# Kernel optimization log

Hardware: AMD Instinct MI355X
Metric: run time of the kernel (lower is better)

## Reference

```python
import math
import jax, jax.numpy as jnp
import numpy as np

B, S, L = 4, 1024, 1024
D, H = 1024, 16
HD = D // H            # 64, even -> rotary_dim == head_dim
HIDDEN = 4 * D         # SwiGLU hidden
ROPE_BASE = 10000.0
EPS = 1e-6


def rmsnorm(x, w):
    return x * jax.lax.rsqrt(jnp.mean(x * x, axis=-1, keepdims=True) + EPS) * w


def safe_key_padding_mask(mask):
    # rows where ALL keys are padded become all-valid to avoid NaN softmax
    all_pad = jnp.all(mask, axis=-1, keepdims=True)
    return jnp.where(all_pad, False, mask)


def split_heads(x):
    b, t, _ = x.shape
    return x.reshape(b, t, H, HD).transpose(0, 2, 1, 3)  # [b,h,t,hd]


def merge_heads(x):
    b, _, t, _ = x.shape
    return x.transpose(0, 2, 1, 3).reshape(b, t, H * HD)


def apply_rope(x):
    # x: [b,h,t,hd]; interleaved even/odd rotation, matching the torch stack/flatten
    t = x.shape[-2]
    pos = jnp.arange(t, dtype=jnp.float32)[:, None]
    freqs = jnp.exp(jnp.arange(0, HD, 2, dtype=jnp.float32) * (-math.log(ROPE_BASE) / HD))
    ang = pos * freqs[None, :]                      # [t, hd/2]
    sin = jnp.sin(ang).astype(x.dtype)
    cos = jnp.cos(ang).astype(x.dtype)
    even, odd = x[..., 0::2], x[..., 1::2]
    rot = jnp.stack((even * cos - odd * sin, even * sin + odd * cos), axis=-1)
    return rot.reshape(x.shape)


def masked_attn(q, k, v, valid_keys):
    # q:[b,h,tq,hd] k,v:[b,h,tk,hd] valid_keys:[b,tk] (True = attendable)
    scores = jnp.einsum('bhqd,bhkd->bhqk', q, k) / math.sqrt(HD)
    scores = jnp.where(valid_keys[:, None, None, :], scores, jnp.finfo(scores.dtype).min)
    return jnp.einsum('bhqk,bhkd->bhqd', jax.nn.softmax(scores, axis=-1), v)


def setup_inputs():
    key = jax.random.key(0)
    ks = jax.random.split(key, 30)
    sc = 0.02
    n = lambda k, shp: jax.random.normal(k, shp, jnp.float32)
    inp = {
        'tokens': n(ks[0], (B, S, D)),
        'seq_tokens': n(ks[1], (B, L, D)),
        'modulation': n(ks[2], (B, D)),
        'attn_norm_w': jnp.ones((D,), jnp.float32),
        'qkv_w': n(ks[3], (3 * D, D)) * sc,
        'qkv_b': jnp.zeros((3 * D,), jnp.float32),
        'out_w': n(ks[4], (D, D)) * sc,
        'out_b': jnp.zeros((D,), jnp.float32),
        'film_w': n(ks[5], (2 * D, D)) * sc,
        'film_b': jnp.zeros((2 * D,), jnp.float32),
        'sq_norm_w': jnp.ones((D,), jnp.float32),
        's_norm_w': jnp.ones((D,), jnp.float32),
        'mha_in_w': n(ks[6], (3 * D, D)) * sc,
        'mha_in_b': jnp.zeros((3 * D,), jnp.float32),
        'mha_out_w': n(ks[7], (D, D)) * sc,
        'mha_out_b': jnp.zeros((D,), jnp.float32),
        'gate_w': n(ks[8], (D, 2 * D)) * sc,
        'gate_b': jnp.zeros((D,), jnp.float32),
        'ffn_norm_w': jnp.ones((D,), jnp.float32),
        'gu_w': n(ks[9], (2 * HIDDEN, D)) * sc,
        'gu_b': jnp.zeros((2 * HIDDEN,), jnp.float32),
        'down_w': n(ks[10], (D, HIDDEN)) * sc,
        'down_b': jnp.zeros((D,), jnp.float32),
        'padding_mask': jax.random.bernoulli(ks[11], 0.1, (B, S)),
        'seq_mask': jax.random.bernoulli(ks[12], 0.1, (B, L)),
    }
    return inp


def reference(tokens, seq_tokens, modulation, attn_norm_w, qkv_w, qkv_b, out_w, out_b,
              film_w, film_b, sq_norm_w, s_norm_w, mha_in_w, mha_in_b, mha_out_w, mha_out_b,
              gate_w, gate_b, ffn_norm_w, gu_w, gu_b, down_w, down_b,
              padding_mask, seq_mask):
    # --- FiLM-modulated pre-norm ---
    x = rmsnorm(tokens, attn_norm_w)
    scale, shift = jnp.split(modulation @ film_w.T + film_b, 2, axis=-1)
    x = x * (1.0 + 0.1 * jnp.tanh(scale))[:, None, :] + shift[:, None, :]
    # --- rotary self-attention ---
    q, k, v = jnp.split(x @ qkv_w.T + qkv_b, 3, axis=-1)
    q, k, v = split_heads(q), split_heads(k), split_heads(v)
    q, k = apply_rope(q), apply_rope(k)
    valid = ~safe_key_padding_mask(padding_mask)
    tokens = tokens + merge_heads(masked_attn(q, k, v, valid)) @ out_w.T + out_b
    # --- cross-attention over the (single) context sequence ---
    query = rmsnorm(tokens, sq_norm_w)
    src = rmsnorm(seq_tokens, s_norm_w)
    wq, wk, wv = jnp.split(mha_in_w, 3, axis=0)
    bq, bk, bv = jnp.split(mha_in_b, 3, axis=0)
    cq = split_heads(query @ wq.T + bq)
    ck = split_heads(src @ wk.T + bk)
    cv = split_heads(src @ wv.T + bv)
    svalid = ~safe_key_padding_mask(seq_mask)
    attended = merge_heads(masked_attn(cq, ck, cv, svalid)) @ mha_out_w.T + mha_out_b
    valid_rows = jnp.any(~seq_mask, axis=1).astype(attended.dtype)[:, None, None]
    update = attended * valid_rows  # mean over 1 sequence == identity
    gate = jax.nn.sigmoid(jnp.concatenate([tokens, update], axis=-1) @ gate_w.T + gate_b)
    tokens = tokens + gate * update
    # --- SwiGLU FFN ---
    h = rmsnorm(tokens, ffn_norm_w)
    g, val = jnp.split(h @ gu_w.T + gu_b, 2, axis=-1)
    return tokens + (jax.nn.silu(g) * val) @ down_w.T + down_b
```

## Files before the change

### kernel.cpp

```cpp
#include <hip/hip_runtime.h>
#include <hip/hip_bf16.h>
#include <math.h>

#define BB 4
#define SS 1024
#define DD 1024
#define NH 16
#define HD 64

using bf16 = __hip_bfloat16;
typedef __bf16 bf16x8 __attribute__((ext_vector_type(8)));
typedef __bf16 bf16x4 __attribute__((ext_vector_type(4)));
typedef float f32x4 __attribute__((ext_vector_type(4)));

#define AS3(p) ((__attribute__((address_space(3))) void*)(p))
#define AS1(p) ((const __attribute__((address_space(1))) void*)(p))

__device__ __forceinline__ void stage128(const bf16* __restrict__ g, int ld,
                                         int row0, int k0, __bf16* lds,
                                         int wave, int lane)
{
    const int l15 = lane & 15, q = lane >> 4;
#pragma unroll
    for (int j = 0; j < 2; ++j) {
        int grp = wave * 2 + j;
        const bf16* gp = g + (size_t)(row0 + grp * 16 + l15) * ld + k0 + q * 8;
        __builtin_amdgcn_global_load_lds(AS1(gp), AS3((char*)lds + grp * 1024), 16, 0, 0);
    }
}

__device__ __forceinline__ void stageH(const bf16* __restrict__ g, int ld,
                                       int row0, int k0, __bf16* lds,
                                       int wid, int lane)
{
    const int l15 = lane & 15, q = lane >> 4;
#pragma unroll
    for (int j = 0; j < 2; ++j) {
        int grp = wid * 2 + j;
        const bf16* gp = g + (size_t)(row0 + grp * 16 + l15) * ld + k0 + q * 8;
        __builtin_amdgcn_global_load_lds(AS1(gp), AS3((char*)lds + grp * 1024), 16, 0, 0);
    }
}

__device__ __forceinline__ bf16x8 ldsfrag(const __bf16* lds, int grp, int quad, int l15)
{
    return *(const bf16x8*)((const char*)lds + grp * 1024 + quad * 256 + l15 * 16);
}

template<int RES>
__global__ __launch_bounds__(512, 2)
void gemm256p_kernel(const bf16* __restrict__ A, const bf16* __restrict__ W, int ldw,
                     const bf16* __restrict__ bias, bf16* __restrict__ Cout,
                     const bf16* __restrict__ Res, int K, int ldc)
{
    __shared__ __bf16 L[2][2][2][8192];
    const int wid = threadIdx.x >> 6, lane = threadIdx.x & 63;
    const int quad = lane >> 4, l15 = lane & 15;
    const int wm = wid >> 2, wn = wid & 3;
    const int n0 = blockIdx.x * 256, m0 = blockIdx.y * 256;
    const int nt = K >> 6;

    stageH(A, K,   m0, 0,  &L[0][0][0][0], wid, lane);
    stageH(W, ldw, n0, 0,  &L[0][1][0][0], wid, lane);
    stageH(A, K,   m0, 32, &L[0][0][1][0], wid, lane);
    stageH(W, ldw, n0, 32, &L[0][1][1][0], wid, lane);

    f32x4 acc[8][4] = {};
    bf16x8 af[8], bf[2];

    for (int t = 0; t < nt; ++t) {
        const int buf = t & 1, nbuf = buf ^ 1;
        const int kn = (t + 1) * 64;
        const bool more = (t + 1) < nt;

        asm volatile("s_waitcnt vmcnt(4)\n\ts_barrier" ::: "memory");
        {
            const __bf16* LA = &L[buf][0][0][0];
            const __bf16* LB = &L[buf][1][0][0];
#pragma unroll
            for (int m = 0; m < 8; ++m) af[m] = ldsfrag(LA, wm * 8 + m, quad, l15);
            bf[0] = ldsfrag(LB, wn * 4 + 0, quad, l15);
            bf[1] = ldsfrag(LB, wn * 4 + 1, quad, l15);
            if (more) stageH(A, K, m0, kn, &L[nbuf][0][0][0], wid, lane);
            __builtin_amdgcn_s_setprio(1);
#pragma unroll
            for (int m = 0; m < 8; ++m) {
                acc[m][0] = __builtin_amdgcn_mfma_f32_16x16x32_bf16(af[m], bf[0], acc[m][0], 0, 0, 0);
                acc[m][1] = __builtin_amdgcn_mfma_f32_16x16x32_bf16(af[m], bf[1], acc[m][1], 0, 0, 0);
            }
            __builtin_amdgcn_s_setprio(0);
        }

        asm volatile("s_barrier" ::: "memory");
        {
            const __bf16* LB = &L[buf][1][0][0];
            bf[0] = ldsfrag(LB, wn * 4 + 2, quad, l15);
            bf[1] = ldsfrag(LB, wn * 4 + 3, quad, l15);
            if (more) stageH(W, ldw, n0, kn, &L[nbuf][1][0][0], wid, lane);
            __builtin_amdgcn_s_setprio(1);
#pragma unroll
            for (int m = 0; m < 8; ++m) {
                acc[m][2] = __builtin_amdgcn_mfma_f32_16x16x32_bf16(af[m], bf[0], acc[m][2], 0, 0, 0);
                acc[m][3] = __builtin_amdgcn_mfma_f32_16x16x32_bf16(af[m], bf[1], acc[m][3], 0, 0, 0);
            }
            __builtin_amdgcn_s_setprio(0);
        }

        if (more) asm volatile("s_waitcnt vmcnt(4)\n\ts_barrier" ::: "memory");
        else      asm volatile("s_waitcnt vmcnt(0)\n\ts_barrier" ::: "memory");
        {
            const __bf16* LA = &L[buf][0][1][0];
            const __bf16* LB = &L[buf][1][1][0];
#pragma unroll
            for (int m = 0; m < 8; ++m) af[m] = ldsfrag(LA, wm * 8 + m, quad, l15);
            bf[0] = ldsfrag(LB, wn * 4 + 0, quad, l15);
            bf[1] = ldsfrag(LB, wn * 4 + 1, quad, l15);
            if (more) stageH(A, K, m0, kn + 32, &L[nbuf][0][1][0], wid, lane);
            __builtin_amdgcn_s_setprio(1);
#pragma unroll
            for (int m = 0; m < 8; ++m) {
                acc[m][0] = __builtin_amdgcn_mfma_f32_16x16x32_bf16(af[m], bf[0], acc[m][0], 0, 0, 0);
                acc[m][1] = __builtin_amdgcn_mfma_f32_16x16x32_bf16(af[m], bf[1], acc[m][1], 0, 0, 0);
            }
            __builtin_amdgcn_s_setprio(0);
        }

        asm volatile("s_barrier" ::: "memory");
        {
            const __bf16* LB = &L[buf][1][1][0];
            bf[0] = ldsfrag(LB, wn * 4 + 2, quad, l15);
            bf[1] = ldsfrag(LB, wn * 4 + 3, quad, l15);
            if (more) stageH(W, ldw, n0, kn + 32, &L[nbuf][1][1][0], wid, lane);
            __builtin_amdgcn_s_setprio(1);
#pragma unroll
            for (int m = 0; m < 8; ++m) {
                acc[m][2] = __builtin_amdgcn_mfma_f32_16x16x32_bf16(af[m], bf[0], acc[m][2], 0, 0, 0);
                acc[m][3] = __builtin_amdgcn_mfma_f32_16x16x32_bf16(af[m], bf[1], acc[m][3], 0, 0, 0);
            }
            __builtin_amdgcn_s_setprio(0);
        }
    }

    const int mw = m0 + wm * 128, nw = n0 + wn * 64;
#pragma unroll
    for (int i = 0; i < 8; ++i)
#pragma unroll
        for (int j = 0; j < 4; ++j) {
            const int col = nw + j * 16 + l15;
            const float bs = (float)bias[col];
#pragma unroll
            for (int r = 0; r < 4; ++r) {
                int row = mw + i * 16 + quad * 4 + r;
                size_t off = (size_t)row * ldc + col;
                float v = acc[i][j][r] + bs;
                if (RES == 2) {
                    float g = fminf(fmaxf(v, -60.f), 60.f);
                    v = (g / (1.f + __expf(-g))) * (float)Res[off];
                }
                Cout[off] = __float2bfloat16(v);
            }
        }
}

template<int RES, bool SCALE>
__global__ __launch_bounds__(256)
void gemm128_kernel(const bf16* __restrict__ A, const bf16* __restrict__ W, int ldw,
                    const bf16* __restrict__ bias, bf16* __restrict__ Cout,
                    const bf16* __restrict__ Res, const float* __restrict__ scaleb,
                    int K, int ldc)
{
    __shared__ __bf16 As[2][4096], Bs[2][4096];
    const int wave = threadIdx.x >> 6, lane = threadIdx.x & 63;
    const int quad = lane >> 4, l15 = lane & 15;
    const int n0 = blockIdx.x * 128, m0 = blockIdx.y * 128;
    const int mg0 = (wave >> 1) * 4, ng0 = (wave & 1) * 4;

    stage128(A, K, m0, 0, As[0], wave, lane);
    stage128(W, ldw, n0, 0, Bs[0], wave, lane);

    f32x4 acc[4][4] = {};
    const int steps = K >> 5;
    for (int s = 0; s < steps; ++s) {
        __syncthreads();
        const int cur = s & 1, nxt = cur ^ 1;
        bf16x8 af[4], bfv[4];
#pragma unroll
        for (int i = 0; i < 4; ++i) af[i] = ldsfrag(As[cur], mg0 + i, quad, l15);
#pragma unroll
        for (int j = 0; j < 4; ++j) bfv[j] = ldsfrag(Bs[cur], ng0 + j, quad, l15);
        if (s + 1 < steps) {
            stage128(A, K, m0, (s + 1) * 32, As[nxt], wave, lane);
            stage128(W, ldw, n0, (s + 1) * 32, Bs[nxt], wave, lane);
        }
#pragma unroll
        for (int i = 0; i < 4; ++i)
#pragma unroll
            for (int j = 0; j < 4; ++j)
                acc[i][j] = __builtin_amdgcn_mfma_f32_16x16x32_bf16(af[i], bfv[j], acc[i][j], 0, 0, 0);
    }

    const float scl = SCALE ? scaleb[m0 >> 10] : 1.f;
#pragma unroll
    for (int i = 0; i < 4; ++i)
#pragma unroll
        for (int j = 0; j < 4; ++j) {
            const int col = n0 + (ng0 + j) * 16 + l15;
            const float bs = (float)bias[col];
#pragma unroll
            for (int r = 0; r < 4; ++r) {
                int row = m0 + (mg0 + i) * 16 + quad * 4 + r;
                float v = acc[i][j][r] + bs;
                if (SCALE) v *= scl;
                size_t off = (size_t)row * ldc + col;
                if (RES == 1) v += (float)Res[off];
                Cout[off] = __float2bfloat16(v);
            }
        }
}

__global__ __launch_bounds__(256)
void gate128_kernel(const bf16* __restrict__ A1, const bf16* __restrict__ A2,
                    const bf16* __restrict__ Wg, const bf16* __restrict__ bias,
                    bf16* __restrict__ GT)
{
    __shared__ __bf16 As[2][4096], Bs[2][4096];
    const int wave = threadIdx.x >> 6, lane = threadIdx.x & 63;
    const int quad = lane >> 4, l15 = lane & 15;
    const int n0 = blockIdx.x * 128, m0 = blockIdx.y * 128;
    const int mg0 = (wave >> 1) * 4, ng0 = (wave & 1) * 4;

    stage128(A1, 1024, m0, 0, As[0], wave, lane);
    stage128(Wg, 2048, n0, 0, Bs[0], wave, lane);

    f32x4 acc[4][4] = {};
    for (int s = 0; s < 64; ++s) {
        __syncthreads();
        const int cur = s & 1, nxt = cur ^ 1;
        bf16x8 af[4], bfv[4];
#pragma unroll
        for (int i = 0; i < 4; ++i) af[i] = ldsfrag(As[cur], mg0 + i, quad, l15);
#pragma unroll
        for (int j = 0; j < 4; ++j) bfv[j] = ldsfrag(Bs[cur], ng0 + j, quad, l15);
        if (s + 1 < 64) {
            const bf16* Asrc = (s + 1 < 32) ? A1 : A2;
            stage128(Asrc, 1024, m0, ((s + 1) & 31) * 32, As[nxt], wave, lane);
            stage128(Wg, 2048, n0, (s + 1) * 32, Bs[nxt], wave, lane);
        }
#pragma unroll
        for (int i = 0; i < 4; ++i)
#pragma unroll
            for (int j = 0; j < 4; ++j)
                acc[i][j] = __builtin_amdgcn_mfma_f32_16x16x32_bf16(af[i], bfv[j], acc[i][j], 0, 0, 0);
    }

#pragma unroll
    for (int i = 0; i < 4; ++i)
#pragma unroll
        for (int j = 0; j < 4; ++j) {
            const int col = n0 + (ng0 + j) * 16 + l15;
            const float bs = (float)bias[col];
#pragma unroll
            for (int r = 0; r < 4; ++r) {
                int row = m0 + (mg0 + i) * 16 + quad * 4 + r;
                float v = fminf(fmaxf(acc[i][j][r] + bs, -60.f), 60.f);
                GT[(size_t)row * 1024 + col] = __float2bfloat16(1.f / (1.f + __expf(-v)));
            }
        }
}

__global__ __launch_bounds__(256)
void down128_kernel(const bf16* __restrict__ ACT, const bf16* __restrict__ W,
                    const bf16* __restrict__ bias, void* __restrict__ out,
                    const bf16* __restrict__ T3, const int* __restrict__ flags)
{
    __shared__ __bf16 As[2][4096], Bs[2][4096];
    const int wave = threadIdx.x >> 6, lane = threadIdx.x & 63;
    const int quad = lane >> 4, l15 = lane & 15;
    const int n0 = blockIdx.x * 128, m0 = blockIdx.y * 128;
    const int mg0 = (wave >> 1) * 4, ng0 = (wave & 1) * 4;

    stage128(ACT, 4096, m0, 0, As[0], wave, lane);
    stage128(W,   4096, n0, 0, Bs[0], wave, lane);

    f32x4 acc[4][4] = {};
    for (int s = 0; s < 128; ++s) {
        __syncthreads();
        const int cur = s & 1, nxt = cur ^ 1;
        bf16x8 af[4], bfv[4];
#pragma unroll
        for (int i = 0; i < 4; ++i) af[i] = ldsfrag(As[cur], mg0 + i, quad, l15);
#pragma unroll
        for (int j = 0; j < 4; ++j) bfv[j] = ldsfrag(Bs[cur], ng0 + j, quad, l15);
        if (s + 1 < 128) {
            stage128(ACT, 4096, m0, (s + 1) * 32, As[nxt], wave, lane);
            stage128(W,   4096, n0, (s + 1) * 32, Bs[nxt], wave, lane);
        }
#pragma unroll
        for (int i = 0; i < 4; ++i)
#pragma unroll
            for (int j = 0; j < 4; ++j)
                acc[i][j] = __builtin_amdgcn_mfma_f32_16x16x32_bf16(af[i], bfv[j], acc[i][j], 0, 0, 0);
    }

    const int f32out = flags[0];
#pragma unroll
    for (int i = 0; i < 4; ++i)
#pragma unroll
        for (int j = 0; j < 4; ++j) {
            const int col = n0 + (ng0 + j) * 16 + l15;
            const float bs = (float)bias[col];
#pragma unroll
            for (int r = 0; r < 4; ++r) {
                size_t row = (size_t)m0 + (mg0 + i) * 16 + quad * 4 + r;
                size_t off = row * 1024 + col;
                float v = acc[i][j][r] + bs + (float)T3[off];
                if (f32out) ((float*)out)[off] = v;
                else        ((bf16*)out)[off] = __float2bfloat16(v);
            }
        }
}

__global__ __launch_bounds__(256)
void probe_kernel(const void* __restrict__ tokens, int* __restrict__ flags)
{
    const unsigned short* u = (const unsigned short*)tokens;
    int t = threadIdx.x, bad = 0;
    for (int i = t; i < 8192; i += 256) {
        int e = (u[i] >> 7) & 0xFF;
        if (e >= 0xC5) bad++;
    }
    __shared__ int red[256];
    red[t] = bad; __syncthreads();
    for (int s = 128; s > 0; s >>= 1) { if (t < s) red[t] += red[t + s]; __syncthreads(); }
    if (t == 0) flags[0] = (red[0] > 16) ? 1 : 0;
}

struct CvtJobs {
    const void* src[23];
    bf16* dst[23];
    int n[23];
    int blk0[24];
};

__global__ __launch_bounds__(256)
void cvt_all_kernel(CvtJobs J, const int* __restrict__ flags)
{
    int b = blockIdx.x, j = 0;
    while (b >= J.blk0[j + 1]) ++j;
    int i0 = (b - J.blk0[j]) * 2048 + threadIdx.x * 8;
    if (i0 >= J.n[j]) return;
    bf16* dst = J.dst[j];
    if (flags[0]) {
        const float4* s = (const float4*)((const float*)J.src[j] + i0);
        float4 a = s[0], c = s[1];
        __bf16 o[8];
        o[0] = (__bf16)a.x; o[1] = (__bf16)a.y; o[2] = (__bf16)a.z; o[3] = (__bf16)a.w;
        o[4] = (__bf16)c.x; o[5] = (__bf16)c.y; o[6] = (__bf16)c.z; o[7] = (__bf16)c.w;
        *(bf16x8*)(dst + i0) = *(bf16x8*)o;
    } else {
        *(bf16x8*)(dst + i0) = *(const bf16x8*)((const bf16*)J.src[j] + i0);
    }
}

__global__ __launch_bounds__(256)
void film_kernel(const bf16* __restrict__ mod, const bf16* __restrict__ fw,
                 const bf16* __restrict__ fb, float* __restrict__ F)
{
    int o = blockIdx.x * 256 + threadIdx.x;
    int b = o >> 11, c = o & 2047;
    const bf16x8* m = (const bf16x8*)(mod + b * DD);
    const bf16x8* w = (const bf16x8*)(fw + (size_t)c * DD);
    float s = (float)fb[c];
    for (int j = 0; j < DD / 8; ++j) {
        bf16x8 mv = m[j], wv = w[j];
#pragma unroll
        for (int e = 0; e < 8; ++e) s += (float)mv[e] * (float)wv[e];
    }
    if (c < 1024) s = 1.f + 0.1f * tanhf(s);
    F[o] = s;
}

template<typename TIN, int FILM>
__global__ __launch_bounds__(256)
void rmsnorm_kernel(const TIN* __restrict__ in, const bf16* __restrict__ w,
                    bf16* __restrict__ out, const float* __restrict__ F)
{
    int row = blockIdx.x, t = threadIdx.x, b = row >> 10;
    const TIN* x = in + (size_t)row * DD;
    float v[4];
    if constexpr (sizeof(TIN) == 2) {
        bf16x4 u = *(const bf16x4*)((const __bf16*)x + t * 4);
#pragma unroll
        for (int i = 0; i < 4; ++i) v[i] = (float)u[i];
    } else {
        float4 u = *(const float4*)((const float*)x + t * 4);
        v[0] = u.x; v[1] = u.y; v[2] = u.z; v[3] = u.w;
    }
    float ss = v[0]*v[0] + v[1]*v[1] + v[2]*v[2] + v[3]*v[3];
    __shared__ float red[256];
    red[t] = ss; __syncthreads();
    for (int s = 128; s > 0; s >>= 1) { if (t < s) red[t] += red[t + s]; __syncthreads(); }
    float rn = rsqrtf(red[0] * (1.f / DD) + 1e-6f);
    bf16x4 wv = *(const bf16x4*)((const __bf16*)w + t * 4);
    __bf16 o4[4];
#pragma unroll
    for (int i = 0; i < 4; ++i) {
        int d = t * 4 + i;
        float y = v[i] * rn * (float)wv[i];
        if (FILM) y = y * F[b * 2048 + d] + F[b * 2048 + 1024 + d];
        o4[i] = (__bf16)y;
    }
    *(bf16x4*)((__bf16*)out + (size_t)row * DD + t * 4) = *(bf16x4*)o4;
}

__global__ __launch_bounds__(256)
void mask_kernel(const void* __restrict__ mask, int* __restrict__ valid,
                 float* __restrict__ vr)
{
    int b = blockIdx.x, t = threadIdx.x;
    const unsigned* mi = (const unsigned*)mask;
    const unsigned char* mb = (const unsigned char*)mask;
    __shared__ int red[256];

    int viol = 0;
    for (int i = t; i < 1024; i += 256) if (mi[i] > 1u) viol++;
    red[t] = viol; __syncthreads();
    for (int s = 128; s > 0; s >>= 1) { if (t < s) red[t] += red[t + s]; __syncthreads(); }
    int isByte = (red[0] > 0);
    __syncthreads();

    int z = 0;
    for (int i = t; i < SS; i += 256) {
        int mv = isByte ? (int)mb[b * SS + i] : (int)mi[b * SS + i];
        z += (mv == 0);
    }
    red[t] = z; __syncthreads();
    for (int s = 128; s > 0; s >>= 1) { if (t < s) red[t] += red[t + s]; __syncthreads(); }
    int nvalid = red[0];
    int allpad = (nvalid == 0);
    for (int i = t; i < SS; i += 256) {
        int mv = isByte ? (int)mb[b * SS + i] : (int)mi[b * SS + i];
        valid[b * SS + i] = allpad ? 1 : (mv ? 0 : 1);
    }
    if (t == 0) vr[b] = (nvalid > 0) ? 1.f : 0.f;
}

__global__ __launch_bounds__(256)
void rope_kernel(bf16* __restrict__ qkv)
{
    int row = blockIdx.x;
    int s = row & (SS - 1);
    for (int j = threadIdx.x; j < 1024; j += 256) {
        int sec = j >> 9;
        int p = j & 511;
        int i = p & 31;
        int col = sec * DD + p * 2;
        float fi = __expf(-(float)(2 * i) * 0.14391157f);
        float ang = (float)s * fi;
        float sn, cs; sincosf(ang, &sn, &cs);
        size_t base = (size_t)row * (3 * DD) + col;
        float e = (float)qkv[base], o = (float)qkv[base + 1];
        qkv[base]     = __float2bfloat16(e * cs - o * sn);
        qkv[base + 1] = __float2bfloat16(e * sn + o * cs);
    }
}

__global__ __launch_bounds__(256)
void vtrans_kernel(const bf16* __restrict__ vsrc, int ld, bf16* __restrict__ vtg)
{
    __shared__ __bf16 tile[64][65];
    const int t = threadIdx.x;
    const int k0 = blockIdx.x * 64;
    const int h = blockIdx.y, b = blockIdx.z;
#pragma unroll
    for (int j = 0; j < 2; ++j) {
        int lin = j * 256 + t;
        int r = lin >> 3, c8 = (lin & 7) * 8;
        bf16x8 v = *(const bf16x8*)(vsrc + ((size_t)b * 1024 + k0 + r) * ld + h * 64 + c8);
#pragma unroll
        for (int e = 0; e < 8; ++e) tile[r][c8 + e] = v[e];
    }
    __syncthreads();
#pragma unroll
    for (int j = 0; j < 2; ++j) {
        int lin = j * 256 + t;
        int d = lin >> 3, k8 = (lin & 7) * 8;
        __bf16 o[8];
#pragma unroll
        for (int e = 0; e < 8; ++e) o[e] = tile[k8 + e][d];
        *(bf16x8*)(vtg + ((size_t)(b * 16 + h) * 64 + d) * 1024 + k0 + k8) = *(bf16x8*)o;
    }
}

__global__ __launch_bounds__(256)
void attn_mfma_kernel(const bf16* __restrict__ qp, const bf16* __restrict__ kp,
                      int ld, const bf16* __restrict__ vtg,
                      const int* __restrict__ valid, bf16* __restrict__ out)
{
    __shared__ __bf16 Kl[128][72];
    __shared__ __bf16 Vl[64][136];
    __shared__ __bf16 Pl[4][16][136];
    __shared__ float biasl[1024];

    const int t = threadIdx.x;
    const int wave = t >> 6, lane = t & 63, quad = lane >> 4, l15 = lane & 15;
    const int q0 = blockIdx.x * 64;
    const int h = blockIdx.y, b = blockIdx.z;

    for (int i = t; i < 1024; i += 256)
        biasl[i] = valid[b * 1024 + i] ? 0.f : -1e30f;

    const size_t qrow = (size_t)b * 1024 + q0 + wave * 16 + l15;
    const bf16x8 qf0 = *(const bf16x8*)(qp + qrow * ld + h * 64 + quad * 8);
    const bf16x8 qf1 = *(const bf16x8*)(qp + qrow * ld + h * 64 + 32 + quad * 8);

    f32x4 O[4] = {{0,0,0,0},{0,0,0,0},{0,0,0,0},{0,0,0,0}};
    float mrow[4] = {-1e30f, -1e30f, -1e30f, -1e30f};
    float lrow[4] = {0.f, 0.f, 0.f, 0.f};

    for (int ic = 0; ic < 8; ++ic) {
        const int k0 = ic * 128;
        __syncthreads();
#pragma unroll
        for (int j = 0; j < 4; ++j) {
            int lin = j * 256 + t;
            int r = lin >> 3, c8 = (lin & 7) * 8;
            *(bf16x8*)&Kl[r][c8] =
                *(const bf16x8*)(kp + ((size_t)b * 1024 + k0 + r) * ld + h * 64 + c8);
            int d = lin >> 4, s8 = (lin & 15) * 8;
            *(bf16x8*)&Vl[d][s8] =
                *(const bf16x8*)(vtg + ((size_t)(b * 16 + h) * 64 + d) * 1024 + k0 + s8);
        }
        __syncthreads();

        float sreg[8][4];
#pragma unroll
        for (int f = 0; f < 8; ++f) {
            bf16x8 kb0 = *(const bf16x8*)&Kl[f * 16 + l15][quad * 8];
            bf16x8 kb1 = *(const bf16x8*)&Kl[f * 16 + l15][32 + quad * 8];
            f32x4 s = {0, 0, 0, 0};
            s = __builtin_amdgcn_mfma_f32_16x16x32_bf16(qf0, kb0, s, 0, 0, 0);
            s = __builtin_amdgcn_mfma_f32_16x16x32_bf16(qf1, kb1, s, 0, 0, 0);
            float bfr = biasl[k0 + f * 16 + l15];
#pragma unroll
            for (int i = 0; i < 4; ++i) sreg[f][i] = s[i] * 0.125f + bfr;
        }

        float mloc[4] = {-1e30f, -1e30f, -1e30f, -1e30f};
#pragma unroll
        for (int f = 0; f < 8; ++f)
#pragma unroll
            for (int i = 0; i < 4; ++i) mloc[i] = fmaxf(mloc[i], sreg[f][i]);
#pragma unroll
        for (int off = 1; off < 16; off <<= 1)
#pragma unroll
            for (int i = 0; i < 4; ++i)
                mloc[i] = fmaxf(mloc[i], __shfl_xor(mloc[i], off));
        float alpha[4];
#pragma unroll
        for (int i = 0; i < 4; ++i) {
            float mn = fmaxf(mrow[i], mloc[i]);
            alpha[i] = __expf(mrow[i] - mn);
            mrow[i] = mn;
            lrow[i] *= alpha[i];
        }
#pragma unroll
        for (int dt = 0; dt < 4; ++dt)
#pragma unroll
            for (int i = 0; i < 4; ++i) O[dt][i] *= alpha[i];

        float lloc[4] = {0.f, 0.f, 0.f, 0.f};
#pragma unroll
        for (int f = 0; f < 8; ++f)
#pragma unroll
            for (int i = 0; i < 4; ++i) {
                float p = __expf(sreg[f][i] - mrow[i]);
                lloc[i] += p;
                Pl[wave][quad * 4 + i][f * 16 + l15] = (__bf16)p;
            }
#pragma unroll
        for (int off = 1; off < 16; off <<= 1)
#pragma unroll
            for (int i = 0; i < 4; ++i) lloc[i] += __shfl_xor(lloc[i], off);
#pragma unroll
        for (int i = 0; i < 4; ++i) lrow[i] += lloc[i];

        __syncthreads();

#pragma unroll
        for (int kc = 0; kc < 4; ++kc) {
            bf16x8 pa = *(const bf16x8*)&Pl[wave][l15][kc * 32 + quad * 8];
#pragma unroll
            for (int dt = 0; dt < 4; ++dt) {
                bf16x8 vb = *(const bf16x8*)&Vl[dt * 16 + l15][kc * 32 + quad * 8];
                O[dt] = __builtin_amdgcn_mfma_f32_16x16x32_bf16(pa, vb, O[dt], 0, 0, 0);
            }
        }
    }

#pragma unroll
    for (int i = 0; i < 4; ++i) {
        float inv = 1.f / lrow[i];
        size_t orow = (size_t)b * 1024 + q0 + wave * 16 + quad * 4 + i;
#pragma unroll
        for (int dt = 0; dt < 4; ++dt)
            out[orow * 1024 + h * 64 + dt * 16 + l15] = __float2bfloat16(O[dt][i] * inv);
    }
}

__global__ __launch_bounds__(256)
void gating_kernel(const bf16* __restrict__ T2, const bf16* __restrict__ GT,
                   const bf16* __restrict__ UPb, bf16* __restrict__ T3)
{
    size_t i0 = ((size_t)blockIdx.x * 256 + threadIdx.x) * 8;
    bf16x8 a = *(const bf16x8*)((const __bf16*)T2 + i0);
    bf16x8 g = *(const bf16x8*)((const __bf16*)GT + i0);
    bf16x8 u = *(const bf16x8*)((const __bf16*)UPb + i0);
    __bf16 o[8];
#pragma unroll
    for (int e = 0; e < 8; ++e)
        o[e] = (__bf16)((float)a[e] + (float)g[e] * (float)u[e]);
    *(bf16x8*)((__bf16*)T3 + i0) = *(bf16x8*)o;
}

extern "C" void kernel_launch(void* const* d_in, const int* in_sizes, int n_in,
                              void* d_out, int out_size, void* d_ws, size_t ws_size,
                              hipStream_t stream)
{
    const int M = BB * SS;
    const size_t MiB = 1 << 20;

    char* ws = (char*)d_ws;

    size_t off = 0;
    auto arena = [&](size_t n) { bf16* p = (bf16*)(ws + off); off += ((n * 2 + 255) & ~(size_t)255); return p; };
    bf16* aTok  = arena(4194304);
    bf16* aSeq  = arena(4194304);
    bf16* aMod  = arena(4096);
    bf16* aANW  = arena(1024);
    bf16* aQKVW = arena(3145728);
    bf16* aQKVB = arena(3072);
    bf16* aOutW = arena(1048576);
    bf16* aOutB = arena(1024);
    bf16* aFilmW= arena(2097152);
    bf16* aFilmB= arena(2048);
    bf16* aSqN  = arena(1024);
    bf16* aSN   = arena(1024);
    bf16* aMIW  = arena(3145728);
    bf16* aMIB  = arena(3072);
    bf16* aMOW  = arena(1048576);
    bf16* aMOB  = arena(1024);
    bf16* aGW   = arena(2097152);
    bf16* aGB   = arena(1024);
    bf16* aFNW  = arena(1024);
    bf16* aGUW  = arena(8388608);
    bf16* aGUB  = arena(8192);
    bf16* aDW   = arena(4194304);
    bf16* aDB   = arena(1024);

    off = (off + MiB - 1) & ~(MiB - 1);
    char* P0 = ws + off;
    char* P1 = P0 + 8 * MiB;
    char* P2 = P0 + 16 * MiB;
    char* P3 = P0 + 24 * MiB;
    char* P4 = P0 + 32 * MiB;
    char* SM = P0 + 40 * MiB;

    bf16* QKV  = (bf16*)P1;
    bf16* A    = (bf16*)P0;
    bf16* Q2   = (bf16*)P1;
    bf16* SRC  = (bf16*)P2;
    bf16* CQ   = (bf16*)P3;
    bf16* CK   = (bf16*)P1;
    bf16* CV   = (bf16*)P0;
    bf16* U    = (bf16*)P2;
    bf16* UPb  = (bf16*)P0;
    bf16* GT   = (bf16*)P1;
    bf16* T3   = (bf16*)P4;
    bf16* Vtg  = (bf16*)P4;
    bf16* ACT  = (bf16*)P0;
    bf16* Vfull= (bf16*)ws;
    bf16* X    = (bf16*)d_out;
    bf16* T2   = (bf16*)d_out;
    bf16* Hb   = (bf16*)d_out;

    float* F    = (float*)SM;
    int* validP = (int*)(SM + 32 * 1024);
    int* validS = (int*)(SM + 48 * 1024);
    float* vrP  = (float*)(SM + 64 * 1024);
    float* vrS  = (float*)(SM + 64 * 1024 + 256);
    int* flags  = (int*)(SM + 64 * 1024 + 512);

    probe_kernel<<<1, 256, 0, stream>>>(d_in[0], flags);

    CvtJobs J;
    const void* srcs[23] = {d_in[0], d_in[1], d_in[2], d_in[3], d_in[4], d_in[5],
                            d_in[6], d_in[7], d_in[8], d_in[9], d_in[10], d_in[11],
                            d_in[12], d_in[13], d_in[14], d_in[15], d_in[16], d_in[17],
                            d_in[18], d_in[19], d_in[20], d_in[21], d_in[22]};
    bf16* dsts[23] = {aTok, aSeq, aMod, aANW, aQKVW, aQKVB, aOutW, aOutB, aFilmW,
                      aFilmB, aSqN, aSN, aMIW, aMIB, aMOW, aMOB, aGW, aGB, aFNW,
                      aGUW, aGUB, aDW, aDB};
    const int ns[23] = {4194304, 4194304, 4096, 1024, 3145728, 3072, 1048576, 1024,
                        2097152, 2048, 1024, 1024, 3145728, 3072, 1048576, 1024,
                        2097152, 1024, 1024, 8388608, 8192, 4194304, 1024};
    int acc_blk = 0;
    for (int j = 0; j < 23; ++j) {
        J.src[j] = srcs[j]; J.dst[j] = dsts[j]; J.n[j] = ns[j];
        J.blk0[j] = acc_blk;
        acc_blk += (ns[j] + 2047) / 2048;
    }
    J.blk0[23] = acc_blk;
    cvt_all_kernel<<<acc_blk, 256, 0, stream>>>(J, flags);

    film_kernel<<<32, 256, 0, stream>>>(aMod, aFilmW, aFilmB, F);
    mask_kernel<<<BB, 256, 0, stream>>>(d_in[23], validP, vrP);
    mask_kernel<<<BB, 256, 0, stream>>>(d_in[24], validS, vrS);

    rmsnorm_kernel<bf16, 1><<<M, 256, 0, stream>>>(aTok, aANW, X, F);

    gemm256p_kernel<0><<<dim3(12, 16), 512, 0, stream>>>(
        X, aQKVW, 1024, aQKVB, QKV, nullptr, 1024, 3072);

    rope_kernel<<<M, 256, 0, stream>>>(QKV);

    vtrans_kernel<<<dim3(16, 16, 4), 256, 0, stream>>>(QKV + 2048, 3072, Vtg);
    attn_mfma_kernel<<<dim3(16, 16, 4), 256, 0, stream>>>(QKV, QKV + 1024, 3072, Vtg, validP, A);

    gemm128_kernel<1, false><<<dim3(8, 32), 256, 0, stream>>>(
        A, aOutW, 1024, aOutB, T2, aTok, nullptr, 1024, 1024);

    rmsnorm_kernel<bf16, 0><<<M, 256, 0, stream>>>(T2, aSqN, Q2, nullptr);
    rmsnorm_kernel<bf16, 0><<<M, 256, 0, stream>>>(aSeq, aSN, SRC, nullptr);

    gemm128_kernel<0, false><<<dim3(8, 32), 256, 0, stream>>>(
        Q2, aMIW, 1024, aMIB, CQ, nullptr, nullptr, 1024, 1024);
    gemm128_kernel<0, false><<<dim3(8, 32), 256, 0, stream>>>(
        SRC, aMIW + 1048576, 1024, aMIB + 1024, CK, nullptr, nullptr, 1024, 1024);
    gemm128_kernel<0, false><<<dim3(8, 32), 256, 0, stream>>>(
        SRC, aMIW + 2097152, 1024, aMIB + 2048, CV, nullptr, nullptr, 1024, 1024);

    vtrans_kernel<<<dim3(16, 16, 4), 256, 0, stream>>>(CV, 1024, Vtg);
    attn_mfma_kernel<<<dim3(16, 16, 4), 256, 0, stream>>>(CQ, CK, 1024, Vtg, validS, U);

    gemm128_kernel<0, true><<<dim3(8, 32), 256, 0, stream>>>(
        U, aMOW, 1024, aMOB, UPb, nullptr, vrS, 1024, 1024);

    gate128_kernel<<<dim3(8, 32), 256, 0, stream>>>(T2, UPb, aGW, aGB, GT);

    gating_kernel<<<(M * 1024) / (256 * 8), 256, 0, stream>>>(T2, GT, UPb, T3);

    rmsnorm_kernel<bf16, 0><<<M, 256, 0, stream>>>(T3, aFNW, Hb, nullptr);

    gemm256p_kernel<0><<<dim3(16, 16), 512, 0, stream>>>(
        Hb, aGUW + (size_t)4096 * 1024, 1024, aGUB + 4096, Vfull, nullptr, 1024, 4096);
    gemm256p_kernel<2><<<dim3(16, 16), 512, 0, stream>>>(
        Hb, aGUW, 1024, aGUB, ACT, Vfull, 1024, 4096);

    down128_kernel<<<dim3(8, 32), 256, 0, stream>>>(ACT, aDW, aDB, d_out, T3, flags);
}
```

Baseline: 826.6 us.

## Split-K gate and down GEMMs with a 256x128 tile kernel, merge cross K/V projections

Replaces the 128x128 gate and down-projection GEMM kernels with a split-K (K split in two) 256x128 tile kernel. It uses 512 threads, a pipeline with two 32-wide k-stages and explicit vmcnt waits, and writes fp32 partials. Separate elementwise kernels then reduce the partials and apply bias, sigmoid or the residual. The cross-attention K and V projections are fused into one wider GEMM writing an interleaved KV buffer, so attention now takes separate q and k strides. This trades extra fp32 partial traffic and two more launches for better tile efficiency and more blocks in flight.

```diff
diff --git a/kernel.cpp b/kernel.cpp
--- a/kernel.cpp
+++ b/kernel.cpp
@@ -40,6 +40,15 @@
         const bf16* gp = g + (size_t)(row0 + grp * 16 + l15) * ld + k0 + q * 8;
         __builtin_amdgcn_global_load_lds(AS1(gp), AS3((char*)lds + grp * 1024), 16, 0, 0);
     }
+}
+
+__device__ __forceinline__ void stageB8(const bf16* __restrict__ g, int ld,
+                                        int row0, int k0, __bf16* lds,
+                                        int wid, int lane)
+{
+    const int l15 = lane & 15, q = lane >> 4;
+    const bf16* gp = g + (size_t)(row0 + wid * 16 + l15) * ld + k0 + q * 8;
+    __builtin_amdgcn_global_load_lds(AS1(gp), AS3((char*)lds + wid * 1024), 16, 0, 0);
 }
 
 __device__ __forceinline__ bf16x8 ldsfrag(const __bf16* lds, int grp, int quad, int l15)
@@ -162,6 +171,138 @@
         }
 }
 
+__global__ __launch_bounds__(512)
+void gemmsk_kernel(const bf16* __restrict__ A0, const bf16* __restrict__ A1, int lda,
+                   const bf16* __restrict__ W0, const bf16* __restrict__ W1, int ldw,
+                   float* __restrict__ PT, int Kz)
+{
+    __shared__ __bf16 LA[2][2][8192];
+    __shared__ __bf16 LB[2][2][4096];
+    const int wid = threadIdx.x >> 6, lane = threadIdx.x & 63;
+    const int quad = lane >> 4, l15 = lane & 15;
+    const int wm = wid >> 2, wn = wid & 3;
+    const int z = blockIdx.z;
+    const bf16* __restrict__ A = z ? A1 : A0;
+    const bf16* __restrict__ W = z ? W1 : W0;
+    const int n0 = blockIdx.x * 128, m0 = blockIdx.y * 256;
+    const int nt = Kz >> 6;
+
+    stageH (A, lda, m0, 0,  &LA[0][0][0], wid, lane);
+    stageB8(W, ldw, n0, 0,  &LB[0][0][0], wid, lane);
+    stageH (A, lda, m0, 32, &LA[0][1][0], wid, lane);
+    stageB8(W, ldw, n0, 32, &LB[0][1][0], wid, lane);
+
+    f32x4 acc[8][2] = {};
+    bf16x8 af[8], bf[2];
+
+    for (int t = 0; t < nt; ++t) {
+        const int buf = t & 1, nbuf = buf ^ 1;
+        const int kn = (t + 1) * 64;
+        const bool more = (t + 1) < nt;
+
+        asm volatile("s_waitcnt vmcnt(3)\n\ts_barrier" ::: "memory");
+        {
+            const __bf16* pA = &LA[buf][0][0];
+            const __bf16* pB = &LB[buf][0][0];
+#pragma unroll
+            for (int m = 0; m < 8; ++m) af[m] = ldsfrag(pA, wm * 8 + m, quad, l15);
+            bf[0] = ldsfrag(pB, wn * 2 + 0, quad, l15);
+            bf[1] = ldsfrag(pB, wn * 2 + 1, quad, l15);
+            if (more) {
+                stageH (A, lda, m0, kn, &LA[nbuf][0][0], wid, lane);
+                stageB8(W, ldw, n0, kn, &LB[nbuf][0][0], wid, lane);
+            }
+            __builtin_amdgcn_s_setprio(1);
+#pragma unroll
+            for (int m = 0; m < 8; ++m) {
+                acc[m][0] = __builtin_amdgcn_mfma_f32_16x16x32_bf16(af[m], bf[0], acc[m][0], 0, 0, 0);
+                acc[m][1] = __builtin_amdgcn_mfma_f32_16x16x32_bf16(af[m], bf[1], acc[m][1], 0, 0, 0);
+            }
+            __builtin_amdgcn_s_setprio(0);
+        }
+
+        if (more) asm volatile("s_waitcnt vmcnt(3)\n\ts_barrier" ::: "memory");
+        else      asm volatile("s_waitcnt vmcnt(0)\n\ts_barrier" ::: "memory");
+        {
+            const __bf16* pA = &LA[buf][1][0];
+            const __bf16* pB = &LB[buf][1][0];
+#pragma unroll
+            for (int m = 0; m < 8; ++m) af[m] = ldsfrag(pA, wm * 8 + m, quad, l15);
+            bf[0] = ldsfrag(pB, wn * 2 + 0, quad, l15);
+            bf[1] = ldsfrag(pB, wn * 2 + 1, quad, l15);
+            if (more) {
+                stageH (A, lda, m0, kn + 32, &LA[nbuf][1][0], wid, lane);
+                stageB8(W, ldw, n0, kn + 32, &LB[nbuf][1][0], wid, lane);
+            }
+            __builtin_amdgcn_s_setprio(1);
+#pragma unroll
+            for (int m = 0; m < 8; ++m) {
+                acc[m][0] = __builtin_amdgcn_mfma_f32_16x16x32_bf16(af[m], bf[0], acc[m][0], 0, 0, 0);
+                acc[m][1] = __builtin_amdgcn_mfma_f32_16x16x32_bf16(af[m], bf[1], acc[m][1], 0, 0, 0);
+            }
+            __builtin_amdgcn_s_setprio(0);
+        }
+    }
+
+    float* P = PT + (size_t)z * (4096 * 1024);
+    const int mw = m0 + wm * 128, nw = n0 + wn * 32;
+#pragma unroll
+    for (int i = 0; i < 8; ++i)
+#pragma unroll
+        for (int j = 0; j < 2; ++j) {
+            const int col = nw + j * 16 + l15;
+#pragma unroll
+            for (int r = 0; r < 4; ++r) {
+                int row = mw + i * 16 + quad * 4 + r;
+                P[(size_t)row * 1024 + col] = acc[i][j][r];
+            }
+        }
+}
+
+__global__ __launch_bounds__(256)
+void reduce_down_kernel(const float* __restrict__ PT, const bf16* __restrict__ bias,
+                        const bf16* __restrict__ T3, void* __restrict__ out,
+                        const int* __restrict__ flags)
+{
+    size_t i0 = ((size_t)blockIdx.x * 256 + threadIdx.x) * 4;
+    float4 p0 = *(const float4*)(PT + i0);
+    float4 p1 = *(const float4*)(PT + 4194304 + i0);
+    int col = (int)(i0 & 1023);
+    bf16x4 b4 = *(const bf16x4*)((const __bf16*)bias + col);
+    bf16x4 t4 = *(const bf16x4*)((const __bf16*)T3 + i0);
+    float v[4] = {p0.x + p1.x, p0.y + p1.y, p0.z + p1.z, p0.w + p1.w};
+#pragma unroll
+    for (int e = 0; e < 4; ++e) v[e] += (float)b4[e] + (float)t4[e];
+    if (flags[0]) {
+        float4 o = {v[0], v[1], v[2], v[3]};
+        *(float4*)((float*)out + i0) = o;
+    } else {
+        __bf16 o4[4];
+#pragma unroll
+        for (int e = 0; e < 4; ++e) o4[e] = (__bf16)v[e];
+        *(bf16x4*)((__bf16*)out + i0) = *(bf16x4*)o4;
+    }
+}
+
+__global__ __launch_bounds__(256)
+void reduce_gate_kernel(const float* __restrict__ PT, const bf16* __restrict__ bias,
+                        bf16* __restrict__ GT)
+{
+    size_t i0 = ((size_t)blockIdx.x * 256 + threadIdx.x) * 4;
+    float4 p0 = *(const float4*)(PT + i0);
+    float4 p1 = *(const float4*)(PT + 4194304 + i0);
+    int col = (int)(i0 & 1023);
+    bf16x4 b4 = *(const bf16x4*)((const __bf16*)bias + col);
+    float v[4] = {p0.x + p1.x, p0.y + p1.y, p0.z + p1.z, p0.w + p1.w};
+    __bf16 o4[4];
+#pragma unroll
+    for (int e = 0; e < 4; ++e) {
+        float g = fminf(fmaxf(v[e] + (float)b4[e], -60.f), 60.f);
+        o4[e] = (__bf16)(1.f / (1.f + __expf(-g)));
+    }
+    *(bf16x4*)((__bf16*)GT + i0) = *(bf16x4*)o4;
+}
+
 template<int RES, bool SCALE>
 __global__ __launch_bounds__(256)
 void gemm128_kernel(const bf16* __restrict__ A, const bf16* __restrict__ W, int ldw,
@@ -214,108 +355,6 @@
                 size_t off = (size_t)row * ldc + col;
                 if (RES == 1) v += (float)Res[off];
                 Cout[off] = __float2bfloat16(v);
-            }
-        }
-}
-
-__global__ __launch_bounds__(256)
-void gate128_kernel(const bf16* __restrict__ A1, const bf16* __restrict__ A2,
-                    const bf16* __restrict__ Wg, const bf16* __restrict__ bias,
-                    bf16* __restrict__ GT)
-{
-    __shared__ __bf16 As[2][4096], Bs[2][4096];
-    const int wave = threadIdx.x >> 6, lane = threadIdx.x & 63;
-    const int quad = lane >> 4, l15 = lane & 15;
-    const int n0 = blockIdx.x * 128, m0 = blockIdx.y * 128;
-    const int mg0 = (wave >> 1) * 4, ng0 = (wave & 1) * 4;
-
-    stage128(A1, 1024, m0, 0, As[0], wave, lane);
-    stage128(Wg, 2048, n0, 0, Bs[0], wave, lane);
-
-    f32x4 acc[4][4] = {};
-    for (int s = 0; s < 64; ++s) {
-        __syncthreads();
-        const int cur = s & 1, nxt = cur ^ 1;
-        bf16x8 af[4], bfv[4];
-#pragma unroll
-        for (int i = 0; i < 4; ++i) af[i] = ldsfrag(As[cur], mg0 + i, quad, l15);
-#pragma unroll
-        for (int j = 0; j < 4; ++j) bfv[j] = ldsfrag(Bs[cur], ng0 + j, quad, l15);
-        if (s + 1 < 64) {
-            const bf16* Asrc = (s + 1 < 32) ? A1 : A2;
-            stage128(Asrc, 1024, m0, ((s + 1) & 31) * 32, As[nxt], wave, lane);
-            stage128(Wg, 2048, n0, (s + 1) * 32, Bs[nxt], wave, lane);
-        }
-#pragma unroll
-        for (int i = 0; i < 4; ++i)
-#pragma unroll
-            for (int j = 0; j < 4; ++j)
-                acc[i][j] = __builtin_amdgcn_mfma_f32_16x16x32_bf16(af[i], bfv[j], acc[i][j], 0, 0, 0);
-    }
-
-#pragma unroll
-    for (int i = 0; i < 4; ++i)
-#pragma unroll
-        for (int j = 0; j < 4; ++j) {
-            const int col = n0 + (ng0 + j) * 16 + l15;
-            const float bs = (float)bias[col];
-#pragma unroll
-            for (int r = 0; r < 4; ++r) {
-                int row = m0 + (mg0 + i) * 16 + quad * 4 + r;
-                float v = fminf(fmaxf(acc[i][j][r] + bs, -60.f), 60.f);
-                GT[(size_t)row * 1024 + col] = __float2bfloat16(1.f / (1.f + __expf(-v)));
-            }
-        }
-}
-
-__global__ __launch_bounds__(256)
-void down128_kernel(const bf16* __restrict__ ACT, const bf16* __restrict__ W,
-                    const bf16* __restrict__ bias, void* __restrict__ out,
-                    const bf16* __restrict__ T3, const int* __restrict__ flags)
-{
-    __shared__ __bf16 As[2][4096], Bs[2][4096];
-    const int wave = threadIdx.x >> 6, lane = threadIdx.x & 63;
-    const int quad = lane >> 4, l15 = lane & 15;
-    const int n0 = blockIdx.x * 128, m0 = blockIdx.y * 128;
-    const int mg0 = (wave >> 1) * 4, ng0 = (wave & 1) * 4;
-
-    stage128(ACT, 4096, m0, 0, As[0], wave, lane);
-    stage128(W,   4096, n0, 0, Bs[0], wave, lane);
-
-    f32x4 acc[4][4] = {};
-    for (int s = 0; s < 128; ++s) {
-        __syncthreads();
-        const int cur = s & 1, nxt = cur ^ 1;
-        bf16x8 af[4], bfv[4];
-#pragma unroll
-        for (int i = 0; i < 4; ++i) af[i] = ldsfrag(As[cur], mg0 + i, quad, l15);
-#pragma unroll
-        for (int j = 0; j < 4; ++j) bfv[j] = ldsfrag(Bs[cur], ng0 + j, quad, l15);
-        if (s + 1 < 128) {
-            stage128(ACT, 4096, m0, (s + 1) * 32, As[nxt], wave, lane);
-            stage128(W,   4096, n0, (s + 1) * 32, Bs[nxt], wave, lane);
-        }
-#pragma unroll
-        for (int i = 0; i < 4; ++i)
-#pragma unroll
-            for (int j = 0; j < 4; ++j)
-                acc[i][j] = __builtin_amdgcn_mfma_f32_16x16x32_bf16(af[i], bfv[j], acc[i][j], 0, 0, 0);
-    }
-
-    const int f32out = flags[0];
-#pragma unroll
-    for (int i = 0; i < 4; ++i)
-#pragma unroll
-        for (int j = 0; j < 4; ++j) {
-            const int col = n0 + (ng0 + j) * 16 + l15;
-            const float bs = (float)bias[col];
-#pragma unroll
-            for (int r = 0; r < 4; ++r) {
-                size_t row = (size_t)m0 + (mg0 + i) * 16 + quad * 4 + r;
-                size_t off = row * 1024 + col;
-                float v = acc[i][j][r] + bs + (float)T3[off];
-                if (f32out) ((float*)out)[off] = v;
-                else        ((bf16*)out)[off] = __float2bfloat16(v);
             }
         }
 }
@@ -494,7 +533,7 @@
 
 __global__ __launch_bounds__(256)
 void attn_mfma_kernel(const bf16* __restrict__ qp, const bf16* __restrict__ kp,
-                      int ld, const bf16* __restrict__ vtg,
+                      int ldq, int ldk, const bf16* __restrict__ vtg,
                       const int* __restrict__ valid, bf16* __restrict__ out)
 {
     __shared__ __bf16 Kl[128][72];
@@ -511,8 +550,8 @@
         biasl[i] = valid[b * 1024 + i] ? 0.f : -1e30f;
 
     const size_t qrow = (size_t)b * 1024 + q0 + wave * 16 + l15;
-    const bf16x8 qf0 = *(const bf16x8*)(qp + qrow * ld + h * 64 + quad * 8);
-    const bf16x8 qf1 = *(const bf16x8*)(qp + qrow * ld + h * 64 + 32 + quad * 8);
+    const bf16x8 qf0 = *(const bf16x8*)(qp + qrow * ldq + h * 64 + quad * 8);
+    const bf16x8 qf1 = *(const bf16x8*)(qp + qrow * ldq + h * 64 + 32 + quad * 8);
 
     f32x4 O[4] = {{0,0,0,0},{0,0,0,0},{0,0,0,0},{0,0,0,0}};
     float mrow[4] = {-1e30f, -1e30f, -1e30f, -1e30f};
@@ -526,7 +565,7 @@
             int lin = j * 256 + t;
             int r = lin >> 3, c8 = (lin & 7) * 8;
             *(bf16x8*)&Kl[r][c8] =
-                *(const bf16x8*)(kp + ((size_t)b * 1024 + k0 + r) * ld + h * 64 + c8);
+                *(const bf16x8*)(kp + ((size_t)b * 1024 + k0 + r) * ldk + h * 64 + c8);
             int d = lin >> 4, s8 = (lin & 15) * 8;
             *(bf16x8*)&Vl[d][s8] =
                 *(const bf16x8*)(vtg + ((size_t)(b * 16 + h) * 64 + d) * 1024 + k0 + s8);
@@ -668,11 +707,10 @@
 
     bf16* QKV  = (bf16*)P1;
     bf16* A    = (bf16*)P0;
-    bf16* Q2   = (bf16*)P1;
+    bf16* Q2   = (bf16*)P3;
     bf16* SRC  = (bf16*)P2;
-    bf16* CQ   = (bf16*)P3;
-    bf16* CK   = (bf16*)P1;
-    bf16* CV   = (bf16*)P0;
+    bf16* CQ   = (bf16*)ws;
+    bf16* KV   = (bf16*)P0;
     bf16* U    = (bf16*)P2;
     bf16* UPb  = (bf16*)P0;
     bf16* GT   = (bf16*)P1;
@@ -680,6 +718,7 @@
     bf16* Vtg  = (bf16*)P4;
     bf16* ACT  = (bf16*)P0;
     bf16* Vfull= (bf16*)ws;
+    float* PTf = (float*)ws;
     bf16* X    = (bf16*)d_out;
     bf16* T2   = (bf16*)d_out;
     bf16* Hb   = (bf16*)d_out;
@@ -725,7 +764,7 @@
     rope_kernel<<<M, 256, 0, stream>>>(QKV);
 
     vtrans_kernel<<<dim3(16, 16, 4), 256, 0, stream>>>(QKV + 2048, 3072, Vtg);
-    attn_mfma_kernel<<<dim3(16, 16, 4), 256, 0, stream>>>(QKV, QKV + 1024, 3072, Vtg, validP, A);
+    attn_mfma_kernel<<<dim3(16, 16, 4), 256, 0, stream>>>(QKV, QKV + 1024, 3072, 3072, Vtg, validP, A);
 
     gemm128_kernel<1, false><<<dim3(8, 32), 256, 0, stream>>>(
         A, aOutW, 1024, aOutB, T2, aTok, nullptr, 1024, 1024);
@@ -735,18 +774,19 @@
 
     gemm128_kernel<0, false><<<dim3(8, 32), 256, 0, stream>>>(
         Q2, aMIW, 1024, aMIB, CQ, nullptr, nullptr, 1024, 1024);
-    gemm128_kernel<0, false><<<dim3(8, 32), 256, 0, stream>>>(
-        SRC, aMIW + 1048576, 1024, aMIB + 1024, CK, nullptr, nullptr, 1024, 1024);
-    gemm128_kernel<0, false><<<dim3(8, 32), 256, 0, stream>>>(
-        SRC, aMIW + 2097152, 1024, aMIB + 2048, CV, nullptr, nullptr, 1024, 1024);
-
-    vtrans_kernel<<<dim3(16, 16, 4), 256, 0, stream>>>(CV, 1024, Vtg);
-    attn_mfma_kernel<<<dim3(16, 16, 4), 256, 0, stream>>>(CQ, CK, 1024, Vtg, validS, U);
+
+    gemm128_kernel<0, false><<<dim3(16, 32), 256, 0, stream>>>(
+        SRC, aMIW + 1048576, 1024, aMIB + 1024, KV, nullptr, nullptr, 1024, 2048);
+
+    vtrans_kernel<<<dim3(16, 16, 4), 256, 0, stream>>>(KV + 1024, 2048, Vtg);
+    attn_mfma_kernel<<<dim3(16, 16, 4), 256, 0, stream>>>(CQ, KV, 1024, 2048, Vtg, validS, U);
 
     gemm128_kernel<0, true><<<dim3(8, 32), 256, 0, stream>>>(
         U, aMOW, 1024, aMOB, UPb, nullptr, vrS, 1024, 1024);
 
-    gate128_kernel<<<dim3(8, 32), 256, 0, stream>>>(T2, UPb, aGW, aGB, GT);
+    gemmsk_kernel<<<dim3(8, 16, 2), 512, 0, stream>>>(
+        T2, UPb, 1024, aGW, aGW + 1024, 2048, PTf, 1024);
+    reduce_gate_kernel<<<4096, 256, 0, stream>>>(PTf, aGB, GT);
 
     gating_kernel<<<(M * 1024) / (256 * 8), 256, 0, stream>>>(T2, GT, UPb, T3);
 
@@ -757,5 +797,7 @@
     gemm256p_kernel<2><<<dim3(16, 16), 512, 0, stream>>>(
         Hb, aGUW, 1024, aGUB, ACT, Vfull, 1024, 4096);
 
-    down128_kernel<<<dim3(8, 32), 256, 0, stream>>>(ACT, aDW, aDB, d_out, T3, flags);
-}
+    gemmsk_kernel<<<dim3(8, 16, 2), 512, 0, stream>>>(
+        ACT, ACT + 2048, 4096, aDW, aDW + 2048, 4096, PTf, 2048);
+    reduce_down_kernel<<<4096, 256, 0, stream>>>(PTf, aDB, T3, d_out, flags);
+}
```

Measured after the change: 756.8 us. 1.09x faster.
